# Optimization experiments

Measured on AMD Instinct MI355X. Metric: run time of the kernel, lower is better.

The kernel has to match this reference:

```python
import jax, jax.numpy as jnp
import numpy as np

B, L, D, HD, DC = 2, 2048, 2048, 64, 2048
NH = D // HD  # 32 heads


def _rms_norm(x, eps):
    return x * jax.lax.rsqrt(jnp.mean(jnp.square(x), axis=-1, keepdims=True) + eps)


def _apply_rope(x, rope):
    # x: [b,h,l,d]; rope: [2,l,d]. x_hat = interleave(-x_odd, x_even)
    x2 = x.reshape(*x.shape[:-1], HD // 2, 2)
    x_hat = jnp.stack([-x2[..., 1], x2[..., 0]], axis=-1).reshape(x.shape)
    return x * rope[0] + x_hat * rope[1]


def setup_inputs() -> dict:
    key = jax.random.key(0)
    ks = jax.random.split(key, 6)
    return {
        "x": jax.random.normal(ks[0], (B, L, D), jnp.float32),
        "condition": jax.random.normal(ks[1], (B, DC), jnp.float32),
        "rope": jax.random.normal(ks[2], (2, L, HD), jnp.float32),
        "w_ada": jax.random.normal(ks[3], (2 * D, DC), jnp.float32) * 0.02,
        "w_qkv": jax.random.normal(ks[4], (3 * D, D), jnp.float32) * 0.02,
        "w_out": jax.random.normal(ks[5], (D, D), jnp.float32) * 0.02,
        "qk_w": jnp.ones((HD,), jnp.float32),
    }


def reference(x, condition, rope, w_ada, w_qkv, w_out, qk_w):
    eps = jnp.finfo(x.dtype).eps
    # AdaRMSNorm
    ss = (condition @ w_ada.T)[:, None, :]          # [b,1,2D]
    shift, scale = jnp.split(ss, 2, axis=-1)
    h = _rms_norm(x, eps) * (1.0 + scale) + shift   # [b,l,D]
    # fused QKV projection: 'b l (n h d)'
    qkv = (h @ w_qkv.T).reshape(B, L, 3, NH, HD)
    qkv = jnp.transpose(qkv, (2, 0, 3, 1, 4))       # [3,b,h,l,d]
    q, k, v = qkv[0], qkv[1], qkv[2]
    # per-head RMSNorm (with affine weight) + RoPE
    q = _apply_rope(_rms_norm(q, eps) * qk_w, rope)
    k = _apply_rope(_rms_norm(k, eps) * qk_w, rope)
    # SDPA
    scores = jnp.einsum('bhqd,bhkd->bhqk', q, k) / jnp.sqrt(jnp.asarray(HD, x.dtype))
    attn = jax.nn.softmax(scores, axis=-1)
    o = jnp.einsum('bhqk,bhkd->bhqd', attn, v)      # [b,h,l,d]
    o = jnp.transpose(o, (0, 2, 1, 3)).reshape(B, L, D)
    return o @ w_out.T
```

## Files before the change

kernel.cpp:

```cpp
#include <hip/hip_runtime.h>


typedef __bf16 bf16x8 __attribute__((ext_vector_type(8)));
typedef float  f32x4  __attribute__((ext_vector_type(4)));
typedef float  f32x16 __attribute__((ext_vector_type(16)));

#define EPS_F32 1.1920929e-07f
#define QSCALE 0.18033688011112042f

#if defined(__has_builtin)
#  if __has_builtin(__builtin_amdgcn_exp2f)
#    define EXP2F(x) __builtin_amdgcn_exp2f(x)
#  else
#    define EXP2F(x) __expf((x) * 0.6931471805599453f)
#  endif
#  if __has_builtin(__builtin_amdgcn_rcpf)
#    define RCPF(x) __builtin_amdgcn_rcpf(x)
#  else
#    define RCPF(x) (1.0f / (x))
#  endif
#else
#  define EXP2F(x) __expf((x) * 0.6931471805599453f)
#  define RCPF(x) (1.0f / (x))
#endif

__device__ __forceinline__ float bf2f(unsigned int u16) {
  union { unsigned int i; float f; } v; v.i = (u16 & 0xffffu) << 16; return v.f;
}
__device__ __forceinline__ unsigned short f2bf(float f) {
  union { float f; unsigned int i; } v; v.f = f;
  unsigned int r = v.i + 0x7fffu + ((v.i >> 16) & 1u);
  return (unsigned short)(r >> 16);
}
__device__ __forceinline__ unsigned int f2bf_rn_u(float f) {
  union { float f; unsigned int i; } v; v.f = f;
  return v.i + 0x8000u;
}

__device__ __forceinline__ void gload16(const void* g, void* l) {
  __builtin_amdgcn_global_load_lds(
      (const __attribute__((address_space(1))) unsigned int*)(unsigned long long)g,
      (__attribute__((address_space(3))) unsigned int*)(unsigned int)(unsigned long long)l,
      16, 0, 0);
}

__global__ __launch_bounds__(256) void ada_gemm_kernel(
    const float* __restrict__ cond, const float* __restrict__ w_ada,
    float* __restrict__ ss)
{
  const int lane = threadIdx.x & 63;
  const int gw = blockIdx.x * 4 + (threadIdx.x >> 6);
  const int b = gw >> 12;
  const int j = gw & 4095;
  const float4* wr = (const float4*)(w_ada + j * 2048);
  const float4* cr = (const float4*)(cond + b * 2048);
  float acc = 0.f;
  #pragma unroll
  for (int k4 = 0; k4 < 8; ++k4) {
    float4 w = wr[lane + k4 * 64];
    float4 c = cr[lane + k4 * 64];
    acc += w.x * c.x + w.y * c.y + w.z * c.z + w.w * c.w;
  }
  #pragma unroll
  for (int off = 1; off < 64; off <<= 1) acc += __shfl_xor(acc, off);
  if (lane == 0) ss[b * 4096 + j] = acc;
}

__global__ __launch_bounds__(256) void ada_rms_kernel(
    const float* __restrict__ x, const float* __restrict__ ss,
    unsigned short* __restrict__ H)
{
  const int row = blockIdx.x;
  const int b = row >> 11;
  const int tid = threadIdx.x;
  const int lane = tid & 63, wave = tid >> 6;
  const float* xr = x + (size_t)row * 2048;
  float4 v0 = ((const float4*)xr)[tid * 2];
  float4 v1 = ((const float4*)xr)[tid * 2 + 1];
  float ssq = v0.x*v0.x + v0.y*v0.y + v0.z*v0.z + v0.w*v0.w
            + v1.x*v1.x + v1.y*v1.y + v1.z*v1.z + v1.w*v1.w;
  #pragma unroll
  for (int off = 1; off < 64; off <<= 1) ssq += __shfl_xor(ssq, off);
  __shared__ float red[4];
  if (lane == 0) red[wave] = ssq;
  __syncthreads();
  const float tot = red[0] + red[1] + red[2] + red[3];
  const float r = rsqrtf(tot * (1.f / 2048.f) + EPS_F32);
  const int c0 = tid * 8;
  const float* sh = ss + b * 4096;
  float xv[8] = {v0.x, v0.y, v0.z, v0.w, v1.x, v1.y, v1.z, v1.w};
  unsigned int pk[4];
  #pragma unroll
  for (int p = 0; p < 4; ++p) {
    const int c = c0 + p * 2;
    float h0 = xv[p*2+0] * r * (1.f + sh[2048 + c])     + sh[c];
    float h1 = xv[p*2+1] * r * (1.f + sh[2048 + c + 1]) + sh[c + 1];
    pk[p] = (unsigned int)f2bf(h0) | ((unsigned int)f2bf(h1) << 16);
  }
  *(uint4*)&H[(size_t)row * 2048 + c0] = make_uint4(pk[0], pk[1], pk[2], pk[3]);
}

__global__ __launch_bounds__(256) void cast2_kernel(
    const float* __restrict__ a,
    const float* __restrict__ b,
    unsigned short* __restrict__ dst)
{
  const int i = blockIdx.x * 256 + threadIdx.x;
  float4 v = (i < 3145728) ? ((const float4*)a)[i]
                           : ((const float4*)b)[i - 3145728];
  unsigned int p0 = (unsigned int)f2bf(v.x) | ((unsigned int)f2bf(v.y) << 16);
  unsigned int p1 = (unsigned int)f2bf(v.z) | ((unsigned int)f2bf(v.w) << 16);
  *(uint2*)&dst[(size_t)i * 4] = make_uint2(p0, p1);
}

template <int MODE>
__global__ __launch_bounds__(256) void gemm_bt_kernel(
    const unsigned short* __restrict__ A,
    const unsigned short* __restrict__ Bw,
    void* __restrict__ Cv,
    unsigned short* __restrict__ vt,
    int M, int N, int K)
{
  __shared__ unsigned short As[128 * 32];
  __shared__ unsigned short Bs[128 * 32];
  const int tid  = threadIdx.x;
  const int lane = tid & 63;
  const int wave = tid >> 6;
  const int wm = (wave >> 1) * 64;
  const int wn = (wave & 1) * 64;
  const int bm = blockIdx.y * 128;
  const int bn = blockIdx.x * 128;

  f32x4 acc[4][4] = {};

  const int sm = tid >> 2;
  const int sk = (tid & 3) * 8;
  const unsigned short* Ap  = A  + (size_t)(bm + sm) * K + sk;
  const unsigned short* Ap2 = Ap + (size_t)64 * K;
  const unsigned short* Bp  = Bw + (size_t)(bn + sm) * K + sk;
  const unsigned short* Bp2 = Bp + (size_t)64 * K;
  unsigned short* lA  = &As[tid * 8];
  unsigned short* lA2 = &As[tid * 8 + 2048];
  unsigned short* lB  = &Bs[tid * 8];
  unsigned short* lB2 = &Bs[tid * 8 + 2048];

  const int fr = lane & 15;
  const int fk = (lane >> 4) * 8;

  for (int k0 = 0; k0 < K; k0 += 32) {
    __syncthreads();
    gload16(Ap  + k0, lA);
    gload16(Ap2 + k0, lA2);
    gload16(Bp  + k0, lB);
    gload16(Bp2 + k0, lB2);
    __syncthreads();

    bf16x8 af[4], bfr[4];
    #pragma unroll
    for (int i = 0; i < 4; ++i)
      af[i] = *(const bf16x8*)&As[(wm + i * 16 + fr) * 32 + fk];
    #pragma unroll
    for (int j = 0; j < 4; ++j)
      bfr[j] = *(const bf16x8*)&Bs[(wn + j * 16 + fr) * 32 + fk];
    #pragma unroll
    for (int i = 0; i < 4; ++i)
      #pragma unroll
      for (int j = 0; j < 4; ++j)
        acc[i][j] = __builtin_amdgcn_mfma_f32_16x16x32_bf16(af[i], bfr[j], acc[i][j], 0, 0, 0);
  }

  const int cr = (lane >> 4) * 4;
  const int cc = lane & 15;
  if (MODE == 2 && bn >= 4096) {
    #pragma unroll
    for (int i = 0; i < 4; ++i)
      #pragma unroll
      for (int j = 0; j < 4; ++j)
        #pragma unroll
        for (int r = 0; r < 4; ++r) {
          const int m  = bm + wm + i * 16 + cr + r;
          const int dg = bn + wn + j * 16 + cc - 4096;
          const int l  = m & 2047;
          const size_t dst = ((size_t)((m >> 11) * 32 + (dg >> 6)) * 64 + (dg & 63)) * 2048
                           + (l >> 6) * 64 + (l & 15) * 4 + ((l >> 4) & 3);
          vt[dst] = f2bf(acc[i][j][r]);
        }
  } else {
    #pragma unroll
    for (int i = 0; i < 4; ++i)
      #pragma unroll
      for (int j = 0; j < 4; ++j)
        #pragma unroll
        for (int r = 0; r < 4; ++r) {
          const int row = bm + wm + i * 16 + cr + r;
          const int col = bn + wn + j * 16 + cc;
          if (MODE != 0)
            ((unsigned short*)Cv)[(size_t)row * N + col] = f2bf(acc[i][j][r]);
          else
            ((float*)Cv)[(size_t)row * N + col] = acc[i][j][r];
        }
  }
}

__global__ __launch_bounds__(512, 2) void gemm_qkv_8p(
    const unsigned short* __restrict__ A,
    const unsigned short* __restrict__ Bw,
    unsigned short* __restrict__ C,
    unsigned short* __restrict__ vt)
{
  __shared__ unsigned short As[2][2][8192];
  __shared__ unsigned short Bs[2][2][8192];

  const int tid  = threadIdx.x;
  const int lane = tid & 63;
  const int wave = tid >> 6;
  const int wrow = (wave >> 2) * 128;
  const int wcol = (wave & 3) * 64;

  const int swz = (blockIdx.x & 7) * 48 + (blockIdx.x >> 3);
  const int bx = swz >> 4;
  const int by = swz & 15;
  const int bm = by * 256;
  const int bn = bx * 256;

  const int fr = lane & 15;
  const int q_ = lane >> 4;
  const int laneoff = fr * 32 + ((q_ ^ ((fr >> 1) & 3)) << 3);

  const int rA  = wave * 32 + (lane >> 2);
  const int kk  = (lane & 3) ^ ((lane >> 3) & 3);
  const unsigned short* Ag0 = A  + (size_t)(bm + rA) * 2048 + kk * 8;
  const unsigned short* Ag1 = Ag0 + (size_t)16 * 2048;
  const unsigned short* Bg0 = Bw + (size_t)(bn + rA) * 2048 + kk * 8;
  const unsigned short* Bg1 = Bg0 + (size_t)16 * 2048;
  const int ldso = rA * 32 + (lane & 3) * 8;

  f32x4 acc[8][4] = {};
  bf16x8 fA[4], fB[4];

#define STAGE_A(SB, SKH, KT) do { \
    gload16(Ag0 + (KT) * 64 + (SKH) * 32, &As[SB][SKH][ldso]); \
    gload16(Ag1 + (KT) * 64 + (SKH) * 32, &As[SB][SKH][ldso + 512]); } while (0)
#define STAGE_B(SB, SKH, KT) do { \
    gload16(Bg0 + (KT) * 64 + (SKH) * 32, &Bs[SB][SKH][ldso]); \
    gload16(Bg1 + (KT) * 64 + (SKH) * 32, &Bs[SB][SKH][ldso + 512]); } while (0)
#define VMW(N) asm volatile("s_waitcnt vmcnt(" #N ")" ::: "memory")
#define LDB(BUF, KH) do { const unsigned short* p_ = &Bs[BUF][KH][wcol * 32 + laneoff]; \
    fB[0] = *(const bf16x8*)&p_[0];    fB[1] = *(const bf16x8*)&p_[512]; \
    fB[2] = *(const bf16x8*)&p_[1024]; fB[3] = *(const bf16x8*)&p_[1536]; } while (0)
#define LDA(BUF, KH, MH) do { const unsigned short* p_ = &As[BUF][KH][(wrow + (MH) * 64) * 32 + laneoff]; \
    fA[0] = *(const bf16x8*)&p_[0];    fA[1] = *(const bf16x8*)&p_[512]; \
    fA[2] = *(const bf16x8*)&p_[1024]; fA[3] = *(const bf16x8*)&p_[1536]; } while (0)
#define MFMA16(MH) do { \
    _Pragma("unroll") \
    for (int f_ = 0; f_ < 4; ++f_) { \
      _Pragma("unroll") \
      for (int n_ = 0; n_ < 4; ++n_) \
        acc[(MH) * 4 + f_][n_] = __builtin_amdgcn_mfma_f32_16x16x32_bf16( \
            fA[f_], fB[n_], acc[(MH) * 4 + f_][n_], 0, 0, 0); \
    } } while (0)
#define PH_MID() do { __builtin_amdgcn_s_barrier(); \
    asm volatile("s_waitcnt lgkmcnt(0)"); \
    __builtin_amdgcn_s_setprio(1); } while (0)
#define PH_END() do { __builtin_amdgcn_s_setprio(0); \
    __builtin_amdgcn_s_barrier(); } while (0)

  STAGE_A(0, 0, 0); STAGE_B(0, 0, 0); STAGE_A(0, 1, 0); STAGE_B(0, 1, 0);
  VMW(4);
  __builtin_amdgcn_s_barrier();

  for (int it = 0; it < 16; ++it) {
    const int t1 = 2 * it + 1;
    const int t2 = 2 * it + 2;
    const bool pf = (it < 15);

    LDB(0, 0); LDA(0, 0, 0);
    STAGE_A(1, 0, t1);
    PH_MID(); MFMA16(0); PH_END();
    LDA(0, 0, 1);
    STAGE_B(1, 0, t1);
    VMW(4);
    PH_MID(); MFMA16(1); PH_END();
    LDB(0, 1); LDA(0, 1, 0);
    STAGE_A(1, 1, t1);
    PH_MID(); MFMA16(0); PH_END();
    LDA(0, 1, 1);
    STAGE_B(1, 1, t1);
    VMW(4);
    PH_MID(); MFMA16(1); PH_END();

    LDB(1, 0); LDA(1, 0, 0);
    if (pf) STAGE_A(0, 0, t2);
    PH_MID(); MFMA16(0); PH_END();
    LDA(1, 0, 1);
    if (pf) { STAGE_B(0, 0, t2); VMW(4); }
    else    { VMW(0); }
    PH_MID(); MFMA16(1); PH_END();
    LDB(1, 1); LDA(1, 1, 0);
    if (pf) STAGE_A(0, 1, t2);
    PH_MID(); MFMA16(0); PH_END();
    LDA(1, 1, 1);
    if (pf) STAGE_B(0, 1, t2);
    VMW(4);
    PH_MID(); MFMA16(1); PH_END();
  }

#undef STAGE_A
#undef STAGE_B
#undef VMW
#undef LDB
#undef LDA
#undef MFMA16
#undef PH_MID
#undef PH_END

  const int cr = (lane >> 4) * 4;
  const int cc = lane & 15;
  if (bn >= 4096) {
    #pragma unroll
    for (int mf = 0; mf < 8; ++mf)
      #pragma unroll
      for (int nf = 0; nf < 4; ++nf)
        #pragma unroll
        for (int r = 0; r < 4; ++r) {
          const int m  = bm + wrow + mf * 16 + cr + r;
          const int dg = bn + wcol + nf * 16 + cc - 4096;
          const int l  = m & 2047;
          const size_t dst = ((size_t)((m >> 11) * 32 + (dg >> 6)) * 64 + (dg & 63)) * 2048
                           + (l >> 6) * 64 + (l & 15) * 4 + ((l >> 4) & 3);
          vt[dst] = f2bf(acc[mf][nf][r]);
        }
  } else {
    #pragma unroll
    for (int mf = 0; mf < 8; ++mf)
      #pragma unroll
      for (int nf = 0; nf < 4; ++nf)
        #pragma unroll
        for (int r = 0; r < 4; ++r) {
          const int row = bm + wrow + mf * 16 + cr + r;
          const int col = bn + wcol + nf * 16 + cc;
          C[(size_t)row * 6144 + col] = f2bf(acc[mf][nf][r]);
        }
  }
}

__global__ __launch_bounds__(256) void qk_rope_kernel(
    unsigned short* __restrict__ QKV, const float* __restrict__ rope,
    const float* __restrict__ qk_w)
{
  const int lane = threadIdx.x & 63;
  const int gid = blockIdx.x * 4 + (threadIdx.x >> 6);
  const int l = gid & 2047;
  const int h = (gid >> 11) & 31;
  const int b = gid >> 16;
  const int base = (b * 2048 + l) * 6144 + h * 64 + lane;
  const float r0 = rope[l * 64 + lane];
  const float r1 = rope[131072 + l * 64 + lane];
  const float w  = qk_w[lane];
  #pragma unroll
  for (int t = 0; t < 2; ++t) {
    const int idx = base + 2048 * t;
    const float v = bf2f(QKV[idx]);
    float sq = v * v;
    #pragma unroll
    for (int off = 1; off < 64; off <<= 1) sq += __shfl_xor(sq, off);
    const float vn = v * rsqrtf(sq * (1.f / 64.f) + EPS_F32) * w;
    const float vp = __shfl_xor(vn, 1);
    const float vh = (lane & 1) ? vp : -vp;
    const float scale = (t == 0) ? QSCALE : 1.0f;
    QKV[idx] = f2bf((vn * r0 + vh * r1) * scale);
  }
}

__global__ __launch_bounds__(256, 2) void attn_mfma_kernel(
    const unsigned short* __restrict__ QKV,
    const unsigned short* __restrict__ Vt,
    unsigned short* __restrict__ O)
{
  __shared__ unsigned short Ks[64 * 72];
  __shared__ unsigned short Vs[64 * 72];
  __shared__ unsigned short Ps[4 * 64 * 68];
  const int tid  = threadIdx.x;
  const int lane = tid & 63;
  const int wave = tid >> 6;
  const int blk = blockIdx.x;
  const int bh = blk & 63;
  const int qt = blk >> 6;
  const int b = bh >> 5, h = bh & 31;
  const int rowbase = b << 11;
  const int qbase = qt * 256 + wave * 64;

  const int m16  = lane & 15;
  const int quad = lane >> 4;
  const int m32  = lane & 31;
  const int hl   = lane >> 5;

  bf16x8 qf[4][2];
  #pragma unroll
  for (int qi = 0; qi < 4; ++qi)
    #pragma unroll
    for (int ch = 0; ch < 2; ++ch)
      qf[qi][ch] = *(const bf16x8*)&QKV[(size_t)(rowbase + qbase + qi * 16 + m16) * 6144
                                        + h * 64 + ch * 32 + quad * 8];

  const int sr = tid >> 2;
  const int sc = (tid & 3) * 16;
  const unsigned short* Kg = QKV + (size_t)(rowbase + sr) * 6144 + 2048 + h * 64 + sc;
  const unsigned short* Vg = Vt + (size_t)(bh * 64 + sr) * 2048 + sc;

  f32x16 accO[2][2] = {};
  float part[4][4] = {};
  unsigned short* Pw = &Ps[(wave * 64) * 68];

  for (int kt = 0; kt < 32; ++kt) {
    __syncthreads();
    {
      const uint4* kp = (const uint4*)(Kg + (size_t)kt * 64 * 6144);
      const uint4* vp = (const uint4*)(Vg + kt * 64);
      uint4 k0 = kp[0], k1 = kp[1];
      uint4 v0 = vp[0], v1 = vp[1];
      *(uint4*)&Ks[sr * 72 + sc]     = k0;
      *(uint4*)&Ks[sr * 72 + sc + 8] = k1;
      *(uint4*)&Vs[sr * 72 + sc]     = v0;
      *(uint4*)&Vs[sr * 72 + sc + 8] = v1;
    }
    __syncthreads();

    unsigned int pk[4][4][2];
    #pragma unroll
    for (int kj = 0; kj < 4; ++kj) {
      bf16x8 kf0 = *(const bf16x8*)&Ks[(kj * 16 + m16) * 72 + quad * 8];
      bf16x8 kf1 = *(const bf16x8*)&Ks[(kj * 16 + m16) * 72 + 32 + quad * 8];
      #pragma unroll
      for (int qi = 0; qi < 4; ++qi) {
        f32x4 acc = {};
        acc = __builtin_amdgcn_mfma_f32_16x16x32_bf16(qf[qi][0], kf0, acc, 0, 0, 0);
        acc = __builtin_amdgcn_mfma_f32_16x16x32_bf16(qf[qi][1], kf1, acc, 0, 0, 0);
        #pragma unroll
        for (int r = 0; r < 4; ++r) {
          float p = EXP2F(acc[r]);
          part[qi][r] += p;
          unsigned int pb = f2bf_rn_u(p);
          if (kj == 0)      pk[qi][r][0]  = pb >> 16;
          else if (kj == 1) pk[qi][r][0] |= pb & 0xffff0000u;
          else if (kj == 2) pk[qi][r][1]  = pb >> 16;
          else              pk[qi][r][1] |= pb & 0xffff0000u;
        }
      }
    }
    #pragma unroll
    for (int qi = 0; qi < 4; ++qi)
      #pragma unroll
      for (int r = 0; r < 4; ++r)
        *(uint2*)&Pw[(qi * 16 + quad * 4 + r) * 68 + m16 * 4] =
            make_uint2(pk[qi][r][0], pk[qi][r][1]);

    #pragma unroll
    for (int ch = 0; ch < 4; ++ch) {
      bf16x8 pa0 = *(const bf16x8*)&Pw[m32 * 68 + ch * 16 + hl * 8];
      bf16x8 pa1 = *(const bf16x8*)&Pw[(32 + m32) * 68 + ch * 16 + hl * 8];
      bf16x8 vb0 = *(const bf16x8*)&Vs[m32 * 72 + ch * 16 + hl * 8];
      bf16x8 vb1 = *(const bf16x8*)&Vs[(32 + m32) * 72 + ch * 16 + hl * 8];
      accO[0][0] = __builtin_amdgcn_mfma_f32_32x32x16_bf16(pa0, vb0, accO[0][0], 0, 0, 0);
      accO[0][1] = __builtin_amdgcn_mfma_f32_32x32x16_bf16(pa0, vb1, accO[0][1], 0, 0, 0);
      accO[1][0] = __builtin_amdgcn_mfma_f32_32x32x16_bf16(pa1, vb0, accO[1][0], 0, 0, 0);
      accO[1][1] = __builtin_amdgcn_mfma_f32_32x32x16_bf16(pa1, vb1, accO[1][1], 0, 0, 0);
    }
  }

  #pragma unroll
  for (int qi = 0; qi < 4; ++qi)
    #pragma unroll
    for (int r = 0; r < 4; ++r)
      #pragma unroll
      for (int off = 1; off < 16; off <<= 1)
        part[qi][r] += __shfl_xor(part[qi][r], off);

  #pragma unroll
  for (int qs = 0; qs < 2; ++qs) {
    #pragma unroll
    for (int reg = 0; reg < 16; ++reg) {
      const int r = reg & 3;
      const int s = reg >> 2;
      const int qsrc = ((2 * s + hl) & 3) * 16 + m16;
      const float rs = __shfl(part[qs * 2 + (reg >> 3)][r], qsrc);
      const float inv = RCPF(rs);
      const int rho = r + 8 * s + 4 * hl;
      const size_t base = (size_t)(rowbase + qbase + qs * 32 + rho) * 2048 + h * 64;
      O[base + m32]      = f2bf(accO[qs][0][reg] * inv);
      O[base + 32 + m32] = f2bf(accO[qs][1][reg] * inv);
    }
  }
}

extern "C" void kernel_launch(void* const* d_in, const int* in_sizes, int n_in,
                              void* d_out, int out_size, void* d_ws, size_t ws_size,
                              hipStream_t stream) {
  (void)in_sizes; (void)n_in; (void)out_size; (void)ws_size;
  const float* x     = (const float*)d_in[0];
  const float* cond  = (const float*)d_in[1];
  const float* rope  = (const float*)d_in[2];
  const float* w_ada = (const float*)d_in[3];
  const float* w_qkv = (const float*)d_in[4];
  const float* w_out = (const float*)d_in[5];
  const float* qk_w  = (const float*)d_in[6];
  float* out = (float*)d_out;

  char* ws = (char*)d_ws;
  float*          ss   = (float*)ws;
  unsigned short* H    = (unsigned short*)(ws + 32768);
  unsigned short* Wq   = H + 8388608;
  unsigned short* Wo   = Wq + 12582912;
  unsigned short* QKV  = Wo + 4194304;
  unsigned short* Vt_g = QKV + 25165824;

  ada_gemm_kernel<<<2048, 256, 0, stream>>>(cond, w_ada, ss);
  ada_rms_kernel<<<4096, 256, 0, stream>>>(x, ss, H);
  cast2_kernel<<<16384, 256, 0, stream>>>(w_qkv, w_out, Wq);
  gemm_qkv_8p<<<384, 512, 0, stream>>>(H, Wq, QKV, Vt_g);
  qk_rope_kernel<<<32768, 256, 0, stream>>>(QKV, rope, qk_w);
  attn_mfma_kernel<<<512, 256, 0, stream>>>(QKV, Vt_g, H);
  gemm_bt_kernel<0><<<dim3(16, 32), 256, 0, stream>>>(H, Wo, (void*)out, nullptr, 4096, 2048, 2048);
}
```

Measured before the change: 467.0 us.

## Double-buffer K/V tiles in attention kernel with register prefetch and setprio

Converts the attention kernel's K/V shared-memory staging to a double buffer. The next tile's global loads are issued into registers before the current tile's compute and written to the alternate buffer afterward, leaving one barrier per iteration instead of two. It also raises wave priority around the MFMA sections via s_setprio. The cost is more LDS, which may affect the two-blocks-per-CU occupancy target, and more live registers for the prefetched data.

```diff
diff --git a/kernel.cpp b/kernel.cpp
--- a/kernel.cpp
+++ b/kernel.cpp
@@ -377,8 +377,8 @@
     const unsigned short* __restrict__ Vt,
     unsigned short* __restrict__ O)
 {
-  __shared__ unsigned short Ks[64 * 72];
-  __shared__ unsigned short Vs[64 * 72];
+  __shared__ unsigned short Ks[2][64 * 72];
+  __shared__ unsigned short Vs[2][64 * 72];
   __shared__ unsigned short Ps[4 * 64 * 68];
   const int tid  = threadIdx.x;
   const int lane = tid & 63;
@@ -407,35 +407,48 @@
   const int sc = (tid & 3) * 16;
   const unsigned short* Kg = QKV + (size_t)(rowbase + sr) * 6144 + 2048 + h * 64 + sc;
   const unsigned short* Vg = Vt + (size_t)(bh * 64 + sr) * 2048 + sc;
+  const int so = sr * 72 + sc;
 
   f32x16 accO[2][2] = {};
   float part[4][4] = {};
   unsigned short* Pw = &Ps[(wave * 64) * 68];
 
+  {
+    const uint4* kp = (const uint4*)Kg;
+    const uint4* vp = (const uint4*)Vg;
+    uint4 k0 = kp[0], k1 = kp[1];
+    uint4 v0 = vp[0], v1 = vp[1];
+    *(uint4*)&Ks[0][so]     = k0;
+    *(uint4*)&Ks[0][so + 8] = k1;
+    *(uint4*)&Vs[0][so]     = v0;
+    *(uint4*)&Vs[0][so + 8] = v1;
+  }
+  __syncthreads();
+
   for (int kt = 0; kt < 32; ++kt) {
-    __syncthreads();
-    {
-      const uint4* kp = (const uint4*)(Kg + (size_t)kt * 64 * 6144);
-      const uint4* vp = (const uint4*)(Vg + kt * 64);
-      uint4 k0 = kp[0], k1 = kp[1];
-      uint4 v0 = vp[0], v1 = vp[1];
-      *(uint4*)&Ks[sr * 72 + sc]     = k0;
-      *(uint4*)&Ks[sr * 72 + sc + 8] = k1;
-      *(uint4*)&Vs[sr * 72 + sc]     = v0;
-      *(uint4*)&Vs[sr * 72 + sc + 8] = v1;
+    const int cur = kt & 1;
+    const bool pf = (kt < 31);
+
+    uint4 nk0, nk1, nv0, nv1;
+    if (pf) {
+      const uint4* kp = (const uint4*)(Kg + (size_t)(kt + 1) * 64 * 6144);
+      const uint4* vp = (const uint4*)(Vg + (kt + 1) * 64);
+      nk0 = kp[0]; nk1 = kp[1];
+      nv0 = vp[0]; nv1 = vp[1];
     }
-    __syncthreads();
 
     unsigned int pk[4][4][2];
     #pragma unroll
     for (int kj = 0; kj < 4; ++kj) {
-      bf16x8 kf0 = *(const bf16x8*)&Ks[(kj * 16 + m16) * 72 + quad * 8];
-      bf16x8 kf1 = *(const bf16x8*)&Ks[(kj * 16 + m16) * 72 + 32 + quad * 8];
+      bf16x8 kf0 = *(const bf16x8*)&Ks[cur][(kj * 16 + m16) * 72 + quad * 8];
+      bf16x8 kf1 = *(const bf16x8*)&Ks[cur][(kj * 16 + m16) * 72 + 32 + quad * 8];
       #pragma unroll
       for (int qi = 0; qi < 4; ++qi) {
         f32x4 acc = {};
+        __builtin_amdgcn_s_setprio(1);
         acc = __builtin_amdgcn_mfma_f32_16x16x32_bf16(qf[qi][0], kf0, acc, 0, 0, 0);
         acc = __builtin_amdgcn_mfma_f32_16x16x32_bf16(qf[qi][1], kf1, acc, 0, 0, 0);
+        __builtin_amdgcn_s_setprio(0);
         #pragma unroll
         for (int r = 0; r < 4; ++r) {
           float p = EXP2F(acc[r]);
@@ -455,17 +468,28 @@
         *(uint2*)&Pw[(qi * 16 + quad * 4 + r) * 68 + m16 * 4] =
             make_uint2(pk[qi][r][0], pk[qi][r][1]);
 
+    __builtin_amdgcn_s_setprio(1);
     #pragma unroll
     for (int ch = 0; ch < 4; ++ch) {
       bf16x8 pa0 = *(const bf16x8*)&Pw[m32 * 68 + ch * 16 + hl * 8];
       bf16x8 pa1 = *(const bf16x8*)&Pw[(32 + m32) * 68 + ch * 16 + hl * 8];
-      bf16x8 vb0 = *(const bf16x8*)&Vs[m32 * 72 + ch * 16 + hl * 8];
-      bf16x8 vb1 = *(const bf16x8*)&Vs[(32 + m32) * 72 + ch * 16 + hl * 8];
+      bf16x8 vb0 = *(const bf16x8*)&Vs[cur][m32 * 72 + ch * 16 + hl * 8];
+      bf16x8 vb1 = *(const bf16x8*)&Vs[cur][(32 + m32) * 72 + ch * 16 + hl * 8];
       accO[0][0] = __builtin_amdgcn_mfma_f32_32x32x16_bf16(pa0, vb0, accO[0][0], 0, 0, 0);
       accO[0][1] = __builtin_amdgcn_mfma_f32_32x32x16_bf16(pa0, vb1, accO[0][1], 0, 0, 0);
       accO[1][0] = __builtin_amdgcn_mfma_f32_32x32x16_bf16(pa1, vb0, accO[1][0], 0, 0, 0);
       accO[1][1] = __builtin_amdgcn_mfma_f32_32x32x16_bf16(pa1, vb1, accO[1][1], 0, 0, 0);
     }
+    __builtin_amdgcn_s_setprio(0);
+
+    if (pf) {
+      const int nxt = cur ^ 1;
+      *(uint4*)&Ks[nxt][so]     = nk0;
+      *(uint4*)&Ks[nxt][so + 8] = nk1;
+      *(uint4*)&Vs[nxt][so]     = nv0;
+      *(uint4*)&Vs[nxt][so + 8] = nv1;
+    }
+    __syncthreads();
   }
 
   #pragma unroll
```

Result: no change. 471.8 us (+1.0%).

## Fuse QK RMSNorm+RoPE into QKV GEMM epilogue and pipeline output GEMM

Applied to the files above, without the earlier changes.

The per-head RMSNorm, qk weight, RoPE and Q scaling move into the QKV GEMM epilogue. The row norm is reduced across the 16 lanes that hold one head's 64 columns. This removes the separate qk_rope kernel and its read-modify-write pass over Q and K. The simple output projection GEMM is replaced by a 256x128-tile, double-buffered, swizzled-LDS kernel with explicit waitcnt/barrier phases and setprio, meant to overlap loads with MFMA. The trade-off is more epilogue work and register pressure in the QKV GEMM, plus a hand-scheduled pipeline that relies on exact vmcnt accounting.

```diff
diff --git a/kernel.cpp b/kernel.cpp
--- a/kernel.cpp
+++ b/kernel.cpp
@@ -113,100 +113,13 @@
   *(uint2*)&dst[(size_t)i * 4] = make_uint2(p0, p1);
 }
 
-template <int MODE>
-__global__ __launch_bounds__(256) void gemm_bt_kernel(
-    const unsigned short* __restrict__ A,
-    const unsigned short* __restrict__ Bw,
-    void* __restrict__ Cv,
-    unsigned short* __restrict__ vt,
-    int M, int N, int K)
-{
-  __shared__ unsigned short As[128 * 32];
-  __shared__ unsigned short Bs[128 * 32];
-  const int tid  = threadIdx.x;
-  const int lane = tid & 63;
-  const int wave = tid >> 6;
-  const int wm = (wave >> 1) * 64;
-  const int wn = (wave & 1) * 64;
-  const int bm = blockIdx.y * 128;
-  const int bn = blockIdx.x * 128;
-
-  f32x4 acc[4][4] = {};
-
-  const int sm = tid >> 2;
-  const int sk = (tid & 3) * 8;
-  const unsigned short* Ap  = A  + (size_t)(bm + sm) * K + sk;
-  const unsigned short* Ap2 = Ap + (size_t)64 * K;
-  const unsigned short* Bp  = Bw + (size_t)(bn + sm) * K + sk;
-  const unsigned short* Bp2 = Bp + (size_t)64 * K;
-  unsigned short* lA  = &As[tid * 8];
-  unsigned short* lA2 = &As[tid * 8 + 2048];
-  unsigned short* lB  = &Bs[tid * 8];
-  unsigned short* lB2 = &Bs[tid * 8 + 2048];
-
-  const int fr = lane & 15;
-  const int fk = (lane >> 4) * 8;
-
-  for (int k0 = 0; k0 < K; k0 += 32) {
-    __syncthreads();
-    gload16(Ap  + k0, lA);
-    gload16(Ap2 + k0, lA2);
-    gload16(Bp  + k0, lB);
-    gload16(Bp2 + k0, lB2);
-    __syncthreads();
-
-    bf16x8 af[4], bfr[4];
-    #pragma unroll
-    for (int i = 0; i < 4; ++i)
-      af[i] = *(const bf16x8*)&As[(wm + i * 16 + fr) * 32 + fk];
-    #pragma unroll
-    for (int j = 0; j < 4; ++j)
-      bfr[j] = *(const bf16x8*)&Bs[(wn + j * 16 + fr) * 32 + fk];
-    #pragma unroll
-    for (int i = 0; i < 4; ++i)
-      #pragma unroll
-      for (int j = 0; j < 4; ++j)
-        acc[i][j] = __builtin_amdgcn_mfma_f32_16x16x32_bf16(af[i], bfr[j], acc[i][j], 0, 0, 0);
-  }
-
-  const int cr = (lane >> 4) * 4;
-  const int cc = lane & 15;
-  if (MODE == 2 && bn >= 4096) {
-    #pragma unroll
-    for (int i = 0; i < 4; ++i)
-      #pragma unroll
-      for (int j = 0; j < 4; ++j)
-        #pragma unroll
-        for (int r = 0; r < 4; ++r) {
-          const int m  = bm + wm + i * 16 + cr + r;
-          const int dg = bn + wn + j * 16 + cc - 4096;
-          const int l  = m & 2047;
-          const size_t dst = ((size_t)((m >> 11) * 32 + (dg >> 6)) * 64 + (dg & 63)) * 2048
-                           + (l >> 6) * 64 + (l & 15) * 4 + ((l >> 4) & 3);
-          vt[dst] = f2bf(acc[i][j][r]);
-        }
-  } else {
-    #pragma unroll
-    for (int i = 0; i < 4; ++i)
-      #pragma unroll
-      for (int j = 0; j < 4; ++j)
-        #pragma unroll
-        for (int r = 0; r < 4; ++r) {
-          const int row = bm + wm + i * 16 + cr + r;
-          const int col = bn + wn + j * 16 + cc;
-          if (MODE != 0)
-            ((unsigned short*)Cv)[(size_t)row * N + col] = f2bf(acc[i][j][r]);
-          else
-            ((float*)Cv)[(size_t)row * N + col] = acc[i][j][r];
-        }
-  }
-}
-
 __global__ __launch_bounds__(512, 2) void gemm_qkv_8p(
     const unsigned short* __restrict__ A,
     const unsigned short* __restrict__ Bw,
     unsigned short* __restrict__ C,
-    unsigned short* __restrict__ vt)
+    unsigned short* __restrict__ vt,
+    const float* __restrict__ rope,
+    const float* __restrict__ qk_w)
 {
   __shared__ unsigned short As[2][2][8192];
   __shared__ unsigned short Bs[2][2][8192];
@@ -331,45 +244,151 @@
           vt[dst] = f2bf(acc[mf][nf][r]);
         }
   } else {
+    const bool is_q = (bn + wcol) < 2048;
+    const float qs = is_q ? QSCALE : 1.0f;
+    float w4[4];
+    #pragma unroll
+    for (int nf = 0; nf < 4; ++nf) w4[nf] = qk_w[nf * 16 + cc];
     #pragma unroll
     for (int mf = 0; mf < 8; ++mf)
       #pragma unroll
-      for (int nf = 0; nf < 4; ++nf)
+      for (int r = 0; r < 4; ++r) {
+        const int row = bm + wrow + mf * 16 + cr + r;
+        const int l = row & 2047;
+        float ssq = 0.f;
         #pragma unroll
-        for (int r = 0; r < 4; ++r) {
-          const int row = bm + wrow + mf * 16 + cr + r;
-          const int col = bn + wcol + nf * 16 + cc;
-          C[(size_t)row * 6144 + col] = f2bf(acc[mf][nf][r]);
+        for (int nf = 0; nf < 4; ++nf) { const float v = acc[mf][nf][r]; ssq += v * v; }
+        ssq += __shfl_xor(ssq, 1);
+        ssq += __shfl_xor(ssq, 2);
+        ssq += __shfl_xor(ssq, 4);
+        ssq += __shfl_xor(ssq, 8);
+        const float rn = rsqrtf(ssq * (1.f / 64.f) + EPS_F32) * qs;
+        const float* rp0 = rope + l * 64 + cc;
+        const float* rp1 = rp0 + 131072;
+        #pragma unroll
+        for (int nf = 0; nf < 4; ++nf) {
+          const float vn = acc[mf][nf][r] * rn * w4[nf];
+          const float vp = __shfl_xor(vn, 1);
+          const float vh = (cc & 1) ? vp : -vp;
+          const float o = vn * rp0[nf * 16] + vh * rp1[nf * 16];
+          C[(size_t)row * 6144 + bn + wcol + nf * 16 + cc] = f2bf(o);
         }
-  }
-}
-
-__global__ __launch_bounds__(256) void qk_rope_kernel(
-    unsigned short* __restrict__ QKV, const float* __restrict__ rope,
-    const float* __restrict__ qk_w)
+      }
+  }
+}
+
+__global__ __launch_bounds__(512, 1) void gemm_out_4p(
+    const unsigned short* __restrict__ A,
+    const unsigned short* __restrict__ Bw,
+    float* __restrict__ C)
 {
-  const int lane = threadIdx.x & 63;
-  const int gid = blockIdx.x * 4 + (threadIdx.x >> 6);
-  const int l = gid & 2047;
-  const int h = (gid >> 11) & 31;
-  const int b = gid >> 16;
-  const int base = (b * 2048 + l) * 6144 + h * 64 + lane;
-  const float r0 = rope[l * 64 + lane];
-  const float r1 = rope[131072 + l * 64 + lane];
-  const float w  = qk_w[lane];
-  #pragma unroll
-  for (int t = 0; t < 2; ++t) {
-    const int idx = base + 2048 * t;
-    const float v = bf2f(QKV[idx]);
-    float sq = v * v;
-    #pragma unroll
-    for (int off = 1; off < 64; off <<= 1) sq += __shfl_xor(sq, off);
-    const float vn = v * rsqrtf(sq * (1.f / 64.f) + EPS_F32) * w;
-    const float vp = __shfl_xor(vn, 1);
-    const float vh = (lane & 1) ? vp : -vp;
-    const float scale = (t == 0) ? QSCALE : 1.0f;
-    QKV[idx] = f2bf((vn * r0 + vh * r1) * scale);
-  }
+  __shared__ unsigned short As[2][2][8192];
+  __shared__ unsigned short Bs[2][2][4096];
+
+  const int tid  = threadIdx.x;
+  const int lane = tid & 63;
+  const int wave = tid >> 6;
+  const int wrow = (wave >> 1) * 64;
+  const int wcol = (wave & 1) * 64;
+
+  const int swz = (blockIdx.x & 7) * 32 + (blockIdx.x >> 3);
+  const int bx = swz >> 4;
+  const int by = swz & 15;
+  const int bm = by * 256;
+  const int bn = bx * 128;
+
+  const int fr = lane & 15;
+  const int q_ = lane >> 4;
+  const int laneoff = fr * 32 + ((q_ ^ ((fr >> 1) & 3)) << 3);
+
+  const int rA = wave * 32 + (lane >> 2);
+  const int rB = wave * 16 + (lane >> 2);
+  const int kk = (lane & 3) ^ ((lane >> 3) & 3);
+  const unsigned short* Ag0 = A  + (size_t)(bm + rA) * 2048 + kk * 8;
+  const unsigned short* Ag1 = Ag0 + (size_t)16 * 2048;
+  const unsigned short* Bg0 = Bw + (size_t)(bn + rB) * 2048 + kk * 8;
+  const int ldsoA = rA * 32 + (lane & 3) * 8;
+  const int ldsoB = rB * 32 + (lane & 3) * 8;
+
+  f32x4 acc[4][4] = {};
+  bf16x8 fA[4], fB[4];
+
+#define STAGE_A4(SB, SKH, KT) do { \
+    gload16(Ag0 + (KT) * 64 + (SKH) * 32, &As[SB][SKH][ldsoA]); \
+    gload16(Ag1 + (KT) * 64 + (SKH) * 32, &As[SB][SKH][ldsoA + 512]); } while (0)
+#define STAGE_B4(SB, SKH, KT) \
+    gload16(Bg0 + (KT) * 64 + (SKH) * 32, &Bs[SB][SKH][ldsoB])
+#define VMW(N) asm volatile("s_waitcnt vmcnt(" #N ")" ::: "memory")
+#define LDB4(BUF, KH) do { const unsigned short* p_ = &Bs[BUF][KH][wcol * 32 + laneoff]; \
+    fB[0] = *(const bf16x8*)&p_[0];    fB[1] = *(const bf16x8*)&p_[512]; \
+    fB[2] = *(const bf16x8*)&p_[1024]; fB[3] = *(const bf16x8*)&p_[1536]; } while (0)
+#define LDA4(BUF, KH) do { const unsigned short* p_ = &As[BUF][KH][wrow * 32 + laneoff]; \
+    fA[0] = *(const bf16x8*)&p_[0];    fA[1] = *(const bf16x8*)&p_[512]; \
+    fA[2] = *(const bf16x8*)&p_[1024]; fA[3] = *(const bf16x8*)&p_[1536]; } while (0)
+#define MFMA16_4() do { \
+    _Pragma("unroll") \
+    for (int f_ = 0; f_ < 4; ++f_) { \
+      _Pragma("unroll") \
+      for (int n_ = 0; n_ < 4; ++n_) \
+        acc[f_][n_] = __builtin_amdgcn_mfma_f32_16x16x32_bf16( \
+            fA[f_], fB[n_], acc[f_][n_], 0, 0, 0); \
+    } } while (0)
+#define PH_MID() do { __builtin_amdgcn_s_barrier(); \
+    asm volatile("s_waitcnt lgkmcnt(0)"); \
+    __builtin_amdgcn_s_setprio(1); } while (0)
+#define PH_END() do { __builtin_amdgcn_s_setprio(0); \
+    __builtin_amdgcn_s_barrier(); } while (0)
+
+  STAGE_A4(0, 0, 0); STAGE_B4(0, 0, 0);
+  STAGE_A4(0, 1, 0); STAGE_B4(0, 1, 0);
+  VMW(3);
+  __builtin_amdgcn_s_barrier();
+
+  for (int it = 0; it < 16; ++it) {
+    const int t1 = 2 * it + 1;
+    const int t2 = 2 * it + 2;
+    const bool pf = (it < 15);
+
+    LDB4(0, 0); LDA4(0, 0);
+    STAGE_A4(1, 0, t1); STAGE_B4(1, 0, t1);
+    VMW(3);
+    PH_MID(); MFMA16_4(); PH_END();
+    LDB4(0, 1); LDA4(0, 1);
+    STAGE_A4(1, 1, t1); STAGE_B4(1, 1, t1);
+    VMW(3);
+    PH_MID(); MFMA16_4(); PH_END();
+
+    LDB4(1, 0); LDA4(1, 0);
+    if (pf) { STAGE_A4(0, 0, t2); STAGE_B4(0, 0, t2); VMW(3); }
+    else    { VMW(0); }
+    PH_MID(); MFMA16_4(); PH_END();
+    LDB4(1, 1); LDA4(1, 1);
+    if (pf) { STAGE_A4(0, 1, t2); STAGE_B4(0, 1, t2); VMW(3); }
+    else    { VMW(0); }
+    PH_MID(); MFMA16_4(); PH_END();
+  }
+
+#undef STAGE_A4
+#undef STAGE_B4
+#undef VMW
+#undef LDB4
+#undef LDA4
+#undef MFMA16_4
+#undef PH_MID
+#undef PH_END
+
+  const int cr = (lane >> 4) * 4;
+  const int cc = lane & 15;
+  #pragma unroll
+  for (int f = 0; f < 4; ++f)
+    #pragma unroll
+    for (int n = 0; n < 4; ++n)
+      #pragma unroll
+      for (int r = 0; r < 4; ++r) {
+        const int row = bm + wrow + f * 16 + cr + r;
+        const int col = bn + wcol + n * 16 + cc;
+        C[(size_t)row * 2048 + col] = acc[f][n][r];
+      }
 }
 
 __global__ __launch_bounds__(256, 2) void attn_mfma_kernel(
@@ -517,8 +536,7 @@
   ada_gemm_kernel<<<2048, 256, 0, stream>>>(cond, w_ada, ss);
   ada_rms_kernel<<<4096, 256, 0, stream>>>(x, ss, H);
   cast2_kernel<<<16384, 256, 0, stream>>>(w_qkv, w_out, Wq);
-  gemm_qkv_8p<<<384, 512, 0, stream>>>(H, Wq, QKV, Vt_g);
-  qk_rope_kernel<<<32768, 256, 0, stream>>>(QKV, rope, qk_w);
+  gemm_qkv_8p<<<384, 512, 0, stream>>>(H, Wq, QKV, Vt_g, rope, qk_w);
   attn_mfma_kernel<<<512, 256, 0, stream>>>(QKV, Vt_g, H);
-  gemm_bt_kernel<0><<<dim3(16, 32), 256, 0, stream>>>(H, Wo, (void*)out, nullptr, 4096, 2048, 2048);
-}
+  gemm_out_4p<<<256, 512, 0, stream>>>(H, Wo, out);
+}
```

New measurement: 447.6 us. 1.04x faster.
